# Performance work log

Measured on AMD Instinct MI355X. Metric: run time of the kernel, lower is better.

## Reference

```python
import jax, jax.numpy as jnp
import numpy as np

EPS = 1e-6

def _ln(x, w, b):
    m = x.mean(-1, keepdims=True)
    v = ((x - m) ** 2).mean(-1, keepdims=True)
    return (x - m) / jnp.sqrt(v + EPS) * w + b

def setup_inputs() -> dict:
    key = jax.random.key(0)
    ks = jax.random.split(key, 16)
    N, P, C, M = 8192, 64, 128, 4096
    MW = M * P  # 262144 gathered tokens
    A, BL = 131072, 65536
    x = jax.random.normal(ks[0], (N, P, C), dtype=jnp.float32)
    index_window = jax.random.permutation(ks[1], N)[:M]
    index_partition = jax.random.permutation(ks[2], MW)
    perm2 = jax.random.permutation(ks[3], MW)
    asy_index = perm2[:A]
    blocked_index = perm2[A:A + BL]
    p = lambda k, sh: 0.02 * jax.random.normal(k, sh, dtype=jnp.float32)
    return {
        "x": x,
        "index_window": index_window,
        "index_partition": index_partition,
        "asy_index": asy_index,
        "blocked_index": blocked_index,
        "M": M,
        "B": N,
        "ln1_w": jnp.ones((C,), jnp.float32), "ln1_b": jnp.zeros((C,), jnp.float32),
        "qkv_w": p(ks[4], (C, 3 * C)), "qkv_b": jnp.zeros((3 * C,), jnp.float32),
        "proj_w": p(ks[5], (C, C)), "proj_b": jnp.zeros((C,), jnp.float32),
        "gamma1": jnp.full((C,), 1e-1, jnp.float32),
        "ln2_w": jnp.ones((C,), jnp.float32), "ln2_b": jnp.zeros((C,), jnp.float32),
        "mlp_w1": p(ks[6], (C, 4 * C)), "mlp_b1": jnp.zeros((4 * C,), jnp.float32),
        "mlp_w2": p(ks[7], (4 * C, C)), "mlp_b2": jnp.zeros((C,), jnp.float32),
        "gamma2": jnp.full((C,), 1e-1, jnp.float32),
    }

def reference(x, index_window, index_partition, asy_index, blocked_index, M, B,
              ln1_w, ln1_b, qkv_w, qkv_b, proj_w, proj_b, gamma1,
              ln2_w, ln2_b, mlp_w1, mlp_b1, mlp_w2, mlp_b2, gamma2):
    N, P, C = x.shape
    H, dh = 4, 32
    scale = dh ** -0.5
    MW = index_partition.shape[0]
    x = _ln(x, ln1_w, ln1_b)                      # first_norm over whole input
    X = x                                          # (N, P, C)
    xw = x[index_window].reshape(-1, C)            # gather windows -> (MW, C)
    XX = xw
    xa = _ln(xw[asy_index], ln1_w, ln1_b)          # second norm on asy tokens
    xw = xw.at[asy_index].set(xa)
    shortcut = xa                                  # (A, C)
    xp = xw[index_partition].reshape(M, -1, C)     # (M, P, C) attention groups
    qkv = (xp @ qkv_w + qkv_b).reshape(M, P, H, 3 * dh).transpose(0, 2, 1, 3)
    q, k, v = jnp.split(qkv, 3, axis=3)            # each (M, H, P, dh)
    attn = jnp.einsum('mhqd,mhkd->mhqk', q, k) * scale
    # scatter scores keyed by key-token into flat map, mask blocked keys, gather back
    am = jnp.zeros((MW, P, H), attn.dtype)
    am = am.at[index_partition].set(jnp.transpose(attn, (0, 3, 2, 1)).reshape(MW, P, H))
    am = am.at[blocked_index].set(-10000.0)
    attn = jnp.transpose(am[index_partition].reshape(M, P, P, H), (0, 3, 2, 1))
    attn = jax.nn.softmax(attn, axis=-1)
    o = jnp.einsum('mhqk,mhkd->mhqd', attn, v).transpose(0, 2, 1, 3).reshape(M, P, C)
    o = o @ proj_w + proj_b
    XX = XX.at[index_partition].set(o.reshape(-1, C))
    y = XX[asy_index]
    # sub_layers: [ls1, droppath(id), ln2, mlp, ls2, droppath(id)]
    y = y * gamma1                                 # i=0
    y = shortcut + y                               # i=1 residual
    shortcut = y
    y2 = _ln(y, ln2_w, ln2_b)                      # i=2
    y2 = jax.nn.gelu(y2 @ mlp_w1 + mlp_b1, approximate=False) @ mlp_w2 + mlp_b2  # i=3
    y2 = y2 * gamma2                               # i=4
    y = shortcut + y2                              # i=5 residual
    XX = XX.at[asy_index].set(y)
    XX = XX.at[blocked_index].set(X[index_window].reshape(-1, C)[blocked_index])
    X = X.at[index_window].set(XX.reshape(M, -1, C))
    return X
```

## Files before the change

### kernel.cpp

```cpp
#include <hip/hip_runtime.h>
#include <hip/hip_bf16.h>
#include <math.h>

#define N_   8192
#define P_   64
#define C_   128
#define M_   4096
#define MW_  (M_ * P_)
#define A_   131072
#define BL_  65536
#define NROWS_ (N_ * P_)

typedef __attribute__((ext_vector_type(8))) __bf16 bf16x8;
typedef __attribute__((ext_vector_type(4))) float f32x4;
typedef __attribute__((ext_vector_type(2))) __bf16 bf16x2;

__device__ __forceinline__ float wave_sum(float v) {
#pragma unroll
  for (int o = 32; o > 0; o >>= 1) v += __shfl_xor(v, o, 64);
  return v;
}

__global__ __launch_bounds__(256) void k_set8(unsigned char* p, int n) {
  int i = blockIdx.x * 256 + threadIdx.x;
  if (i < n) p[i] = 0;
}
__global__ __launch_bounds__(256) void k_scatter2(unsigned char* p,
                                                  const int* __restrict__ ia,
                                                  const int* __restrict__ ib) {
  int i = blockIdx.x * 256 + threadIdx.x;
  if (i < A_) p[ia[i]] = 1;
  else {
    int j = i - A_;
    if (j < BL_) p[ib[j]] = 2;
  }
}

__global__ __launch_bounds__(256) void k_prep(const float* __restrict__ qkvw,
                                              const float* __restrict__ projw,
                                              const float* __restrict__ w1,
                                              const float* __restrict__ w2,
                                              __bf16* __restrict__ qkvt,
                                              __bf16* __restrict__ projt,
                                              __bf16* __restrict__ w1t,
                                              __bf16* __restrict__ w2t) {
  int i = blockIdx.x * 256 + threadIdx.x;
  if (i < 384 * 128) {
    int col = i >> 7, row = i & 127;
    qkvt[i] = (__bf16)qkvw[row * 384 + col];
  } else if (i < 384 * 128 + 128 * 128) {
    int j = i - 384 * 128;
    int col = j >> 7, row = j & 127;
    projt[j] = (__bf16)projw[row * 128 + col];
  } else if (i < 384 * 128 + 128 * 128 + 512 * 128) {
    int j = i - 384 * 128 - 128 * 128;
    int col = j >> 7, row = j & 127;
    w1t[j] = (__bf16)w1[row * 512 + col];
  } else {
    int j = i - 384 * 128 - 128 * 128 - 512 * 128;
    int col = j >> 9, row = j & 511;
    w2t[j] = (__bf16)w2[row * 128 + col];
  }
}

__global__ __launch_bounds__(256) void k_ln_all(const float* __restrict__ x,
                                                const float* __restrict__ w,
                                                const float* __restrict__ b,
                                                float* __restrict__ out) {
  int hw = threadIdx.x >> 5, l = threadIdx.x & 31;
  size_t row = (size_t)blockIdx.x * 8 + hw;
  float4 v = ((const float4*)(x + row * 128))[l];
  float s = (v.x + v.y) + (v.z + v.w);
#pragma unroll
  for (int o = 1; o < 32; o <<= 1) s += __shfl_xor(s, o, 64);
  float mean = s * (1.0f / 128.0f);
  float d0 = v.x - mean, d1 = v.y - mean, d2 = v.z - mean, d3 = v.w - mean;
  float q = (d0 * d0 + d1 * d1) + (d2 * d2 + d3 * d3);
#pragma unroll
  for (int o = 1; o < 32; o <<= 1) q += __shfl_xor(q, o, 64);
  float inv = rsqrtf(q * (1.0f / 128.0f) + 1e-6f);
  float4 wv = ((const float4*)w)[l];
  float4 bv = ((const float4*)b)[l];
  float4 o4;
  o4.x = d0 * inv * wv.x + bv.x;
  o4.y = d1 * inv * wv.y + bv.y;
  o4.z = d2 * inv * wv.z + bv.z;
  o4.w = d3 * inv * wv.w + bv.w;
  ((float4*)(out + row * 128))[l] = o4;
}

__global__ __launch_bounds__(256, 3) void k_attn(
    const int* __restrict__ iw,
    const int* __restrict__ ip, const unsigned char* __restrict__ flags,
    const float* __restrict__ ln1w, const float* __restrict__ ln1b,
    const __bf16* __restrict__ qkvt, const float* __restrict__ qkvb,
    const __bf16* __restrict__ projt, const float* __restrict__ projb,
    float* out) {
  __shared__ __align__(16) __bf16 XV[64 * 132];
  __shared__ __align__(16) __bf16 scratch[4 * 4352];
  __shared__ int srow[64];
  __shared__ unsigned char fl[64];

  const int tid = threadIdx.x;
  const int w = tid >> 6, lane = tid & 63;
  const int quad = lane >> 4, cl = lane & 15;
  const int m = blockIdx.x;

  if (tid < 64) {
    int s = ip[(m << 6) + tid];
    fl[tid] = flags[s];
    srow[tid] = iw[s >> 6] * 64 + (s & 63);
  }
  __syncthreads();

  __bf16* Xs = XV;
  const float lw0 = ln1w[2 * lane], lw1 = ln1w[2 * lane + 1];
  const float lb0 = ln1b[2 * lane], lb1 = ln1b[2 * lane + 1];

  {
    float2 xv[16];
#pragma unroll
    for (int ii = 0; ii < 16; ++ii) {
      int r = w + 4 * ii;
      xv[ii] = ((const float2*)(out + (size_t)srow[r] * 128))[lane];
    }
#pragma unroll
    for (int ii = 0; ii < 16; ++ii) {
      int r = w + 4 * ii;
      float y0 = xv[ii].x, y1 = xv[ii].y;
      if (fl[r] == 1) {
        float mean = wave_sum(y0 + y1) * (1.0f / 128.0f);
        float d0 = y0 - mean, d1 = y1 - mean;
        float inv = rsqrtf(wave_sum(d0 * d0 + d1 * d1) * (1.0f / 128.0f) + 1e-6f);
        y0 = d0 * inv * lw0 + lb0;
        y1 = d1 * inv * lw1 + lb1;
      }
      bf16x2 p2;
      p2[0] = (__bf16)y0; p2[1] = (__bf16)y1;
      *(bf16x2*)&Xs[r * 132 + 2 * lane] = p2;
    }
  }
  __syncthreads();

  __bf16* wsc = scratch + w * 4352;
  __bf16* Qs  = wsc;
  __bf16* Ks  = wsc + 2176;
  __bf16* Vts = XV + w * 2112;
  __bf16* Ps  = wsc;
  __bf16* Os  = wsc;
  const int h = w;

  bf16x8 af[4][4];
#pragma unroll
  for (int mt = 0; mt < 4; ++mt)
#pragma unroll
    for (int kt = 0; kt < 4; ++kt)
      af[mt][kt] = *(const bf16x8*)&Xs[(mt * 16 + cl) * 132 + kt * 32 + quad * 8];
  __syncthreads();

#pragma unroll
  for (int t = 0; t < 3; ++t) {
#pragma unroll
    for (int nt = 0; nt < 2; ++nt) {
      int col = h * 96 + t * 32 + nt * 16 + cl;
      bf16x8 bfr[4];
#pragma unroll
      for (int kt = 0; kt < 4; ++kt)
        bfr[kt] = *(const bf16x8*)&qkvt[(size_t)col * 128 + kt * 32 + quad * 8];
      float bias = qkvb[col];
      __builtin_amdgcn_s_setprio(1);
#pragma unroll
      for (int mt = 0; mt < 4; ++mt) {
        f32x4 acc = {bias, bias, bias, bias};
#pragma unroll
        for (int kt = 0; kt < 4; ++kt)
          acc = __builtin_amdgcn_mfma_f32_16x16x32_bf16(af[mt][kt], bfr[kt], acc, 0, 0, 0);
        if (t == 0) {
#pragma unroll
          for (int r = 0; r < 4; ++r)
            Qs[(mt * 16 + quad * 4 + r) * 34 + nt * 16 + cl] = (__bf16)acc[r];
        } else if (t == 1) {
#pragma unroll
          for (int r = 0; r < 4; ++r)
            Ks[(mt * 16 + quad * 4 + r) * 34 + nt * 16 + cl] = (__bf16)acc[r];
        } else {
#pragma unroll
          for (int r = 0; r < 4; ++r)
            Vts[(nt * 16 + cl) * 66 + mt * 16 + quad * 4 + r] = (__bf16)acc[r];
        }
      }
      __builtin_amdgcn_s_setprio(0);
    }
  }

  f32x4 sc4[4][4];
  {
    bf16x8 bk[4];
#pragma unroll
    for (int nt = 0; nt < 4; ++nt)
      bk[nt] = *(const bf16x8*)&Ks[(nt * 16 + cl) * 34 + quad * 8];
    __builtin_amdgcn_s_setprio(1);
#pragma unroll
    for (int mt = 0; mt < 4; ++mt) {
      bf16x8 aq = *(const bf16x8*)&Qs[(mt * 16 + cl) * 34 + quad * 8];
#pragma unroll
      for (int nt = 0; nt < 4; ++nt) {
        f32x4 z = {0.f, 0.f, 0.f, 0.f};
        sc4[mt][nt] = __builtin_amdgcn_mfma_f32_16x16x32_bf16(aq, bk[nt], z, 0, 0, 0);
      }
    }
    __builtin_amdgcn_s_setprio(0);
  }
  const float scale = 0.17677669529663687f;
  bool blk[4];
#pragma unroll
  for (int nt = 0; nt < 4; ++nt) blk[nt] = (fl[nt * 16 + cl] == 2);
#pragma unroll
  for (int mt = 0; mt < 4; ++mt)
#pragma unroll
    for (int nt = 0; nt < 4; ++nt)
#pragma unroll
      for (int r = 0; r < 4; ++r) {
        float v = sc4[mt][nt][r];
        sc4[mt][nt][r] = blk[nt] ? -10000.0f : v * scale;
      }
#pragma unroll
  for (int mt = 0; mt < 4; ++mt) {
#pragma unroll
    for (int r = 0; r < 4; ++r) {
      float mx = fmaxf(fmaxf(sc4[mt][0][r], sc4[mt][1][r]),
                       fmaxf(sc4[mt][2][r], sc4[mt][3][r]));
#pragma unroll
      for (int off = 1; off < 16; off <<= 1) mx = fmaxf(mx, __shfl_xor(mx, off, 64));
      float e0 = __expf(sc4[mt][0][r] - mx);
      float e1 = __expf(sc4[mt][1][r] - mx);
      float e2 = __expf(sc4[mt][2][r] - mx);
      float e3 = __expf(sc4[mt][3][r] - mx);
      float sm = (e0 + e1) + (e2 + e3);
#pragma unroll
      for (int off = 1; off < 16; off <<= 1) sm += __shfl_xor(sm, off, 64);
      float inv = 1.0f / sm;
      int row = mt * 16 + quad * 4 + r;
      Ps[row * 68 +  0 + cl] = (__bf16)(e0 * inv);
      Ps[row * 68 + 16 + cl] = (__bf16)(e1 * inv);
      Ps[row * 68 + 32 + cl] = (__bf16)(e2 * inv);
      Ps[row * 68 + 48 + cl] = (__bf16)(e3 * inv);
    }
  }

  f32x4 oacc[4][2];
  {
    bf16x8 bv[2][2];
#pragma unroll
    for (int nt = 0; nt < 2; ++nt)
#pragma unroll
      for (int kt = 0; kt < 2; ++kt)
        bv[nt][kt] = *(const bf16x8*)&Vts[(nt * 16 + cl) * 66 + kt * 32 + quad * 8];
    __builtin_amdgcn_s_setprio(1);
#pragma unroll
    for (int mt = 0; mt < 4; ++mt) {
      bf16x8 ap0 = *(const bf16x8*)&Ps[(mt * 16 + cl) * 68 + quad * 8];
      bf16x8 ap1 = *(const bf16x8*)&Ps[(mt * 16 + cl) * 68 + 32 + quad * 8];
#pragma unroll
      for (int nt = 0; nt < 2; ++nt) {
        f32x4 z = {0.f, 0.f, 0.f, 0.f};
        z = __builtin_amdgcn_mfma_f32_16x16x32_bf16(ap0, bv[nt][0], z, 0, 0, 0);
        z = __builtin_amdgcn_mfma_f32_16x16x32_bf16(ap1, bv[nt][1], z, 0, 0, 0);
        oacc[mt][nt] = z;
      }
    }
    __builtin_amdgcn_s_setprio(0);
  }
#pragma unroll
  for (int mt = 0; mt < 4; ++mt)
#pragma unroll
    for (int nt = 0; nt < 2; ++nt)
#pragma unroll
      for (int r = 0; r < 4; ++r)
        Os[(mt * 16 + quad * 4 + r) * 36 + nt * 16 + cl] = (__bf16)oacc[mt][nt][r];
  __syncthreads();

  const int jw = w * 32;
#pragma unroll
  for (int mt = 0; mt < 4; ++mt) {
#pragma unroll
    for (int nt = 0; nt < 2; ++nt) {
      int col = jw + nt * 16 + cl;
      float pb = projb[col];
      f32x4 acc = {pb, pb, pb, pb};
#pragma unroll
      for (int kt = 0; kt < 4; ++kt) {
        const __bf16* op = scratch + kt * 4352;
        bf16x8 a = *(const bf16x8*)&op[(mt * 16 + cl) * 36 + quad * 8];
        bf16x8 bb = *(const bf16x8*)&projt[(size_t)col * 128 + kt * 32 + quad * 8];
        acc = __builtin_amdgcn_mfma_f32_16x16x32_bf16(a, bb, acc, 0, 0, 0);
      }
#pragma unroll
      for (int r = 0; r < 4; ++r) {
        int row = mt * 16 + quad * 4 + r;
        if (fl[row] != 2)
          out[(size_t)srow[row] * 128 + col] = acc[r];
      }
    }
  }
}

__global__ __launch_bounds__(256, 4) void k_mlp(
    const float* __restrict__ x, const int* __restrict__ iw,
    const int* __restrict__ ia,
    const float* __restrict__ ln1w, const float* __restrict__ ln1b,
    const float* __restrict__ g1,
    const float* __restrict__ ln2w, const float* __restrict__ ln2b,
    const __bf16* __restrict__ w1t, const float* __restrict__ b1,
    const __bf16* __restrict__ w2t, const float* __restrict__ b2,
    const float* __restrict__ g2,
    float* out) {
  __shared__ __align__(16) __bf16 y2s[64 * 136];
  __shared__ __align__(16) __bf16 hb[64 * 136];
  __shared__ int wrs[64];

  const int tid = threadIdx.x;
  const int w = tid >> 6, lane = tid & 63;
  const int quad = lane >> 4, cl = lane & 15;

  if (tid < 64) {
    int s = ia[(blockIdx.x << 6) + tid];
    wrs[tid] = iw[s >> 6] * 64 + (s & 63);
  }
  __syncthreads();

  const float lw0 = ln1w[2 * lane], lw1 = ln1w[2 * lane + 1];
  const float lb0 = ln1b[2 * lane], lb1 = ln1b[2 * lane + 1];
  const float g1a = g1[2 * lane], g1b = g1[2 * lane + 1];
  const float l2w0 = ln2w[2 * lane], l2w1 = ln2w[2 * lane + 1];
  const float l2b0 = ln2b[2 * lane], l2b1 = ln2b[2 * lane + 1];

  for (int half = 0; half < 2; ++half) {
    float2 xv[8], ov[8];
#pragma unroll
    for (int ii = 0; ii < 8; ++ii) {
      int r = w + 4 * (half * 8 + ii);
      size_t wr = (size_t)wrs[r];
      xv[ii] = ((const float2*)(x + wr * 128))[lane];
      ov[ii] = ((const float2*)(out + wr * 128))[lane];
    }
#pragma unroll
    for (int ii = 0; ii < 8; ++ii) {
      int r = w + 4 * (half * 8 + ii);
      float mean = wave_sum(xv[ii].x + xv[ii].y) * (1.0f / 128.0f);
      float d0 = xv[ii].x - mean, d1 = xv[ii].y - mean;
      float inv = rsqrtf(wave_sum(d0 * d0 + d1 * d1) * (1.0f / 128.0f) + 1e-6f);
      float y0 = d0 * inv * lw0 + lb0, y1 = d1 * inv * lw1 + lb1;
      mean = wave_sum(y0 + y1) * (1.0f / 128.0f);
      d0 = y0 - mean; d1 = y1 - mean;
      inv = rsqrtf(wave_sum(d0 * d0 + d1 * d1) * (1.0f / 128.0f) + 1e-6f);
      float xa0 = d0 * inv * lw0 + lb0, xa1 = d1 * inv * lw1 + lb1;
      float yv0 = xa0 + g1a * ov[ii].x;
      float yv1 = xa1 + g1b * ov[ii].y;
      ((float2*)(out + (size_t)wrs[r] * 128))[lane] = make_float2(yv0, yv1);
      mean = wave_sum(yv0 + yv1) * (1.0f / 128.0f);
      d0 = yv0 - mean; d1 = yv1 - mean;
      inv = rsqrtf(wave_sum(d0 * d0 + d1 * d1) * (1.0f / 128.0f) + 1e-6f);
      bf16x2 p2;
      p2[0] = (__bf16)(d0 * inv * l2w0 + l2b0);
      p2[1] = (__bf16)(d1 * inv * l2w1 + l2b1);
      *(bf16x2*)&y2s[r * 136 + 2 * lane] = p2;
    }
  }
  __threadfence_block();
  __syncthreads();

  f32x4 zacc[4][2];
#pragma unroll
  for (int nt = 0; nt < 2; ++nt) {
    float bb = b2[w * 32 + nt * 16 + cl];
#pragma unroll
    for (int mt = 0; mt < 4; ++mt) zacc[mt][nt] = (f32x4){bb, bb, bb, bb};
  }

  for (int ch = 0; ch < 4; ++ch) {
#pragma unroll
    for (int nt = 0; nt < 2; ++nt) {
      int col = ch * 128 + w * 32 + nt * 16 + cl;
      bf16x8 bfr[4];
#pragma unroll
      for (int kt = 0; kt < 4; ++kt)
        bfr[kt] = *(const bf16x8*)&w1t[(size_t)col * 128 + kt * 32 + quad * 8];
      float bias = b1[col];
      __builtin_amdgcn_s_setprio(1);
#pragma unroll
      for (int mt = 0; mt < 4; ++mt) {
        f32x4 acc = {bias, bias, bias, bias};
#pragma unroll
        for (int kt = 0; kt < 4; ++kt) {
          bf16x8 a = *(const bf16x8*)&y2s[(mt * 16 + cl) * 136 + kt * 32 + quad * 8];
          acc = __builtin_amdgcn_mfma_f32_16x16x32_bf16(a, bfr[kt], acc, 0, 0, 0);
        }
#pragma unroll
        for (int r = 0; r < 4; ++r) {
          float a = acc[r];
          float g = a * 0.5f * (1.0f + erff(a * 0.70710678118654752f));
          hb[(mt * 16 + quad * 4 + r) * 136 + w * 32 + nt * 16 + cl] = (__bf16)g;
        }
      }
      __builtin_amdgcn_s_setprio(0);
    }
    __syncthreads();
#pragma unroll
    for (int nt = 0; nt < 2; ++nt) {
      int col = w * 32 + nt * 16 + cl;
      bf16x8 bfr[4];
#pragma unroll
      for (int kk = 0; kk < 4; ++kk)
        bfr[kk] = *(const bf16x8*)&w2t[(size_t)col * 512 + ch * 128 + kk * 32 + quad * 8];
      __builtin_amdgcn_s_setprio(1);
#pragma unroll
      for (int mt = 0; mt < 4; ++mt)
#pragma unroll
        for (int kk = 0; kk < 4; ++kk) {
          bf16x8 a = *(const bf16x8*)&hb[(mt * 16 + cl) * 136 + kk * 32 + quad * 8];
          zacc[mt][nt] = __builtin_amdgcn_mfma_f32_16x16x32_bf16(a, bfr[kk],
                                                                zacc[mt][nt], 0, 0, 0);
        }
      __builtin_amdgcn_s_setprio(0);
    }
    __syncthreads();
  }

#pragma unroll
  for (int mt = 0; mt < 4; ++mt)
#pragma unroll
    for (int nt = 0; nt < 2; ++nt) {
      int col = w * 32 + nt * 16 + cl;
      float gg = g2[col];
#pragma unroll
      for (int r = 0; r < 4; ++r) {
        int row = mt * 16 + quad * 4 + r;
        size_t a = (size_t)wrs[row] * 128 + col;
        out[a] = out[a] + gg * zacc[mt][nt][r];
      }
    }
}

extern "C" void kernel_launch(void* const* d_in, const int* in_sizes, int n_in,
                              void* d_out, int out_size, void* d_ws, size_t ws_size,
                              hipStream_t stream) {
  const float* x = (const float*)d_in[0];
  const int* iw = (const int*)d_in[1];
  const int* ip = (const int*)d_in[2];
  const int* ia = (const int*)d_in[3];
  const int* ib = (const int*)d_in[4];
  const float* ln1w = (const float*)d_in[7];
  const float* ln1b = (const float*)d_in[8];
  const float* qkvw = (const float*)d_in[9];
  const float* qkvb = (const float*)d_in[10];
  const float* projw = (const float*)d_in[11];
  const float* projb = (const float*)d_in[12];
  const float* g1 = (const float*)d_in[13];
  const float* ln2w = (const float*)d_in[14];
  const float* ln2b = (const float*)d_in[15];
  const float* w1 = (const float*)d_in[16];
  const float* b1 = (const float*)d_in[17];
  const float* w2 = (const float*)d_in[18];
  const float* b2 = (const float*)d_in[19];
  const float* g2 = (const float*)d_in[20];
  float* out = (float*)d_out;

  unsigned char* flags = (unsigned char*)d_ws;
  __bf16* qkvt = (__bf16*)((char*)d_ws + MW_);
  __bf16* projt = (__bf16*)((char*)d_ws + MW_ + 384 * 128 * 2);
  __bf16* w1t = (__bf16*)((char*)d_ws + MW_ + 384 * 128 * 2 + 128 * 128 * 2);
  __bf16* w2t = (__bf16*)((char*)d_ws + MW_ + 384 * 128 * 2 + 128 * 128 * 2 + 512 * 128 * 2);

  k_set8<<<MW_ / 256, 256, 0, stream>>>(flags, MW_);
  k_scatter2<<<(A_ + BL_) / 256, 256, 0, stream>>>(flags, ia, ib);
  k_prep<<<(384 * 128 + 128 * 128 + 512 * 128 + 128 * 512) / 256, 256, 0, stream>>>(
      qkvw, projw, w1, w2, qkvt, projt, w1t, w2t);
  k_ln_all<<<NROWS_ / 8, 256, 0, stream>>>(x, ln1w, ln1b, out);
  k_attn<<<M_, 256, 0, stream>>>(iw, ip, flags, ln1w, ln1b, qkvt, qkvb,
                                 projt, projb, out);
  k_mlp<<<A_ / 64, 256, 0, stream>>>(x, iw, ia, ln1w, ln1b, g1, ln2w, ln2b,
                                     w1t, b1, w2t, b2, g2, out);
}
```

Before: 804.3 us.

## Split attention work across 8 waves per block with row-halves per head

The attention kernel moves from 256 to 512 threads per block, and each head's query rows are split across two waves. This halves per-wave registers and MFMA chains, which should raise occupancy and latency hiding. The projection stage now holds its weight fragments in registers, one 16-column slice per wave, instead of reloading them per row tile. In exchange it adds extra block-wide barriers, because the two waves sharing a head's Q/K/P scratch must synchronise before buffers are reused.

```diff
diff --git a/kernel.cpp b/kernel.cpp
--- a/kernel.cpp
+++ b/kernel.cpp
@@ -89,7 +89,7 @@
   ((float4*)(out + row * 128))[l] = o4;
 }
 
-__global__ __launch_bounds__(256, 3) void k_attn(
+__global__ __launch_bounds__(512, 6) void k_attn(
     const int* __restrict__ iw,
     const int* __restrict__ ip, const unsigned char* __restrict__ flags,
     const float* __restrict__ ln1w, const float* __restrict__ ln1b,
@@ -104,6 +104,7 @@
   const int tid = threadIdx.x;
   const int w = tid >> 6, lane = tid & 63;
   const int quad = lane >> 4, cl = lane & 15;
+  const int h = w >> 1, mh = w & 1;
   const int m = blockIdx.x;
 
   if (tid < 64) {
@@ -118,15 +119,15 @@
   const float lb0 = ln1b[2 * lane], lb1 = ln1b[2 * lane + 1];
 
   {
-    float2 xv[16];
-#pragma unroll
-    for (int ii = 0; ii < 16; ++ii) {
-      int r = w + 4 * ii;
+    float2 xv[8];
+#pragma unroll
+    for (int ii = 0; ii < 8; ++ii) {
+      int r = w * 8 + ii;
       xv[ii] = ((const float2*)(out + (size_t)srow[r] * 128))[lane];
     }
 #pragma unroll
-    for (int ii = 0; ii < 16; ++ii) {
-      int r = w + 4 * ii;
+    for (int ii = 0; ii < 8; ++ii) {
+      int r = w * 8 + ii;
       float y0 = xv[ii].x, y1 = xv[ii].y;
       if (fl[r] == 1) {
         float mean = wave_sum(y0 + y1) * (1.0f / 128.0f);
@@ -142,20 +143,19 @@
   }
   __syncthreads();
 
-  __bf16* wsc = scratch + w * 4352;
+  __bf16* wsc = scratch + h * 4352;
   __bf16* Qs  = wsc;
   __bf16* Ks  = wsc + 2176;
-  __bf16* Vts = XV + w * 2112;
+  __bf16* Vts = XV + h * 2112;
   __bf16* Ps  = wsc;
   __bf16* Os  = wsc;
-  const int h = w;
-
-  bf16x8 af[4][4];
-#pragma unroll
-  for (int mt = 0; mt < 4; ++mt)
+
+  bf16x8 af[2][4];
+#pragma unroll
+  for (int mtl = 0; mtl < 2; ++mtl)
 #pragma unroll
     for (int kt = 0; kt < 4; ++kt)
-      af[mt][kt] = *(const bf16x8*)&Xs[(mt * 16 + cl) * 132 + kt * 32 + quad * 8];
+      af[mtl][kt] = *(const bf16x8*)&Xs[((mh * 2 + mtl) * 16 + cl) * 132 + kt * 32 + quad * 8];
   __syncthreads();
 
 #pragma unroll
@@ -170,11 +170,12 @@
       float bias = qkvb[col];
       __builtin_amdgcn_s_setprio(1);
 #pragma unroll
-      for (int mt = 0; mt < 4; ++mt) {
+      for (int mtl = 0; mtl < 2; ++mtl) {
+        int mt = mh * 2 + mtl;
         f32x4 acc = {bias, bias, bias, bias};
 #pragma unroll
         for (int kt = 0; kt < 4; ++kt)
-          acc = __builtin_amdgcn_mfma_f32_16x16x32_bf16(af[mt][kt], bfr[kt], acc, 0, 0, 0);
+          acc = __builtin_amdgcn_mfma_f32_16x16x32_bf16(af[mtl][kt], bfr[kt], acc, 0, 0, 0);
         if (t == 0) {
 #pragma unroll
           for (int r = 0; r < 4; ++r)
@@ -192,55 +193,60 @@
       __builtin_amdgcn_s_setprio(0);
     }
   }
-
-  f32x4 sc4[4][4];
+  __syncthreads();
+
+  f32x4 sc4[2][4];
   {
     bf16x8 bk[4];
 #pragma unroll
     for (int nt = 0; nt < 4; ++nt)
       bk[nt] = *(const bf16x8*)&Ks[(nt * 16 + cl) * 34 + quad * 8];
+    bf16x8 aq[2];
+#pragma unroll
+    for (int mtl = 0; mtl < 2; ++mtl)
+      aq[mtl] = *(const bf16x8*)&Qs[((mh * 2 + mtl) * 16 + cl) * 34 + quad * 8];
     __builtin_amdgcn_s_setprio(1);
 #pragma unroll
-    for (int mt = 0; mt < 4; ++mt) {
-      bf16x8 aq = *(const bf16x8*)&Qs[(mt * 16 + cl) * 34 + quad * 8];
+    for (int mtl = 0; mtl < 2; ++mtl)
 #pragma unroll
       for (int nt = 0; nt < 4; ++nt) {
         f32x4 z = {0.f, 0.f, 0.f, 0.f};
-        sc4[mt][nt] = __builtin_amdgcn_mfma_f32_16x16x32_bf16(aq, bk[nt], z, 0, 0, 0);
-      }
-    }
+        sc4[mtl][nt] = __builtin_amdgcn_mfma_f32_16x16x32_bf16(aq[mtl], bk[nt], z, 0, 0, 0);
+      }
     __builtin_amdgcn_s_setprio(0);
   }
+  __syncthreads();
+
   const float scale = 0.17677669529663687f;
   bool blk[4];
 #pragma unroll
   for (int nt = 0; nt < 4; ++nt) blk[nt] = (fl[nt * 16 + cl] == 2);
 #pragma unroll
-  for (int mt = 0; mt < 4; ++mt)
+  for (int mtl = 0; mtl < 2; ++mtl)
 #pragma unroll
     for (int nt = 0; nt < 4; ++nt)
 #pragma unroll
       for (int r = 0; r < 4; ++r) {
-        float v = sc4[mt][nt][r];
-        sc4[mt][nt][r] = blk[nt] ? -10000.0f : v * scale;
-      }
-#pragma unroll
-  for (int mt = 0; mt < 4; ++mt) {
+        float v = sc4[mtl][nt][r];
+        sc4[mtl][nt][r] = blk[nt] ? -10000.0f : v * scale;
+      }
+#pragma unroll
+  for (int mtl = 0; mtl < 2; ++mtl) {
 #pragma unroll
     for (int r = 0; r < 4; ++r) {
-      float mx = fmaxf(fmaxf(sc4[mt][0][r], sc4[mt][1][r]),
-                       fmaxf(sc4[mt][2][r], sc4[mt][3][r]));
+      float mx = fmaxf(fmaxf(sc4[mtl][0][r], sc4[mtl][1][r]),
+                       fmaxf(sc4[mtl][2][r], sc4[mtl][3][r]));
 #pragma unroll
       for (int off = 1; off < 16; off <<= 1) mx = fmaxf(mx, __shfl_xor(mx, off, 64));
-      float e0 = __expf(sc4[mt][0][r] - mx);
-      float e1 = __expf(sc4[mt][1][r] - mx);
-      float e2 = __expf(sc4[mt][2][r] - mx);
-      float e3 = __expf(sc4[mt][3][r] - mx);
+      float e0 = __expf(sc4[mtl][0][r] - mx);
+      float e1 = __expf(sc4[mtl][1][r] - mx);
+      float e2 = __expf(sc4[mtl][2][r] - mx);
+      float e3 = __expf(sc4[mtl][3][r] - mx);
       float sm = (e0 + e1) + (e2 + e3);
 #pragma unroll
       for (int off = 1; off < 16; off <<= 1) sm += __shfl_xor(sm, off, 64);
       float inv = 1.0f / sm;
-      int row = mt * 16 + quad * 4 + r;
+      int row = (mh * 2 + mtl) * 16 + quad * 4 + r;
       Ps[row * 68 +  0 + cl] = (__bf16)(e0 * inv);
       Ps[row * 68 + 16 + cl] = (__bf16)(e1 * inv);
       Ps[row * 68 + 32 + cl] = (__bf16)(e2 * inv);
@@ -248,7 +254,7 @@
     }
   }
 
-  f32x4 oacc[4][2];
+  f32x4 oacc[2][2];
   {
     bf16x8 bv[2][2];
 #pragma unroll
@@ -258,7 +264,8 @@
         bv[nt][kt] = *(const bf16x8*)&Vts[(nt * 16 + cl) * 66 + kt * 32 + quad * 8];
     __builtin_amdgcn_s_setprio(1);
 #pragma unroll
-    for (int mt = 0; mt < 4; ++mt) {
+    for (int mtl = 0; mtl < 2; ++mtl) {
+      int mt = mh * 2 + mtl;
       bf16x8 ap0 = *(const bf16x8*)&Ps[(mt * 16 + cl) * 68 + quad * 8];
       bf16x8 ap1 = *(const bf16x8*)&Ps[(mt * 16 + cl) * 68 + 32 + quad * 8];
 #pragma unroll
@@ -266,34 +273,36 @@
         f32x4 z = {0.f, 0.f, 0.f, 0.f};
         z = __builtin_amdgcn_mfma_f32_16x16x32_bf16(ap0, bv[nt][0], z, 0, 0, 0);
         z = __builtin_amdgcn_mfma_f32_16x16x32_bf16(ap1, bv[nt][1], z, 0, 0, 0);
-        oacc[mt][nt] = z;
+        oacc[mtl][nt] = z;
       }
     }
     __builtin_amdgcn_s_setprio(0);
   }
-#pragma unroll
-  for (int mt = 0; mt < 4; ++mt)
+  __syncthreads();
+#pragma unroll
+  for (int mtl = 0; mtl < 2; ++mtl)
 #pragma unroll
     for (int nt = 0; nt < 2; ++nt)
 #pragma unroll
       for (int r = 0; r < 4; ++r)
-        Os[(mt * 16 + quad * 4 + r) * 36 + nt * 16 + cl] = (__bf16)oacc[mt][nt][r];
-  __syncthreads();
-
-  const int jw = w * 32;
-#pragma unroll
-  for (int mt = 0; mt < 4; ++mt) {
-#pragma unroll
-    for (int nt = 0; nt < 2; ++nt) {
-      int col = jw + nt * 16 + cl;
-      float pb = projb[col];
+        Os[((mh * 2 + mtl) * 16 + quad * 4 + r) * 36 + nt * 16 + cl] = (__bf16)oacc[mtl][nt][r];
+  __syncthreads();
+
+  {
+    const int col = w * 16 + cl;
+    bf16x8 bpr[4];
+#pragma unroll
+    for (int kt = 0; kt < 4; ++kt)
+      bpr[kt] = *(const bf16x8*)&projt[(size_t)col * 128 + kt * 32 + quad * 8];
+    const float pb = projb[col];
+#pragma unroll
+    for (int mt = 0; mt < 4; ++mt) {
       f32x4 acc = {pb, pb, pb, pb};
 #pragma unroll
       for (int kt = 0; kt < 4; ++kt) {
         const __bf16* op = scratch + kt * 4352;
         bf16x8 a = *(const bf16x8*)&op[(mt * 16 + cl) * 36 + quad * 8];
-        bf16x8 bb = *(const bf16x8*)&projt[(size_t)col * 128 + kt * 32 + quad * 8];
-        acc = __builtin_amdgcn_mfma_f32_16x16x32_bf16(a, bb, acc, 0, 0, 0);
+        acc = __builtin_amdgcn_mfma_f32_16x16x32_bf16(a, bpr[kt], acc, 0, 0, 0);
       }
 #pragma unroll
       for (int r = 0; r < 4; ++r) {
@@ -477,7 +486,7 @@
   k_prep<<<(384 * 128 + 128 * 128 + 512 * 128 + 128 * 512) / 256, 256, 0, stream>>>(
       qkvw, projw, w1, w2, qkvt, projt, w1t, w2t);
   k_ln_all<<<NROWS_ / 8, 256, 0, stream>>>(x, ln1w, ln1b, out);
-  k_attn<<<M_, 256, 0, stream>>>(iw, ip, flags, ln1w, ln1b, qkvt, qkvb,
+  k_attn<<<M_, 512, 0, stream>>>(iw, ip, flags, ln1w, ln1b, qkvt, qkvb,
                                  projt, projb, out);
   k_mlp<<<A_ / 64, 256, 0, stream>>>(x, iw, ia, ln1w, ln1b, g1, ln2w, ln2b,
                                      w1t, b1, w2t, b2, g2, out);
```

New measurement: 838.8 us. 4.3% more time.

## Merge weight prep into LN launch and keep MLP residual and operands on-chip

Applied to the files above, without the earlier changes.

Folds the weight transpose/convert kernel into the first-LayerNorm kernel as extra blocks, removing one launch. In the MLP kernel, the residual row is kept in shared memory instead of being written to and re-read from global memory. The two bf16 LDS buffers become one reused buffer, and the MFMA A-operands are preloaded into registers. Occupancy is lowered to 3 blocks per CU to make room for the extra registers and shared memory.

```diff
diff --git a/kernel.cpp b/kernel.cpp
--- a/kernel.cpp
+++ b/kernel.cpp
@@ -10,6 +10,8 @@
 #define A_   131072
 #define BL_  65536
 #define NROWS_ (N_ * P_)
+#define LNBLK_ (NROWS_ / 8)
+#define PREPBLK_ (196608 / 256)
 
 typedef __attribute__((ext_vector_type(8))) __bf16 bf16x8;
 typedef __attribute__((ext_vector_type(4))) float f32x4;
@@ -36,37 +38,38 @@
   }
 }
 
-__global__ __launch_bounds__(256) void k_prep(const float* __restrict__ qkvw,
-                                              const float* __restrict__ projw,
-                                              const float* __restrict__ w1,
-                                              const float* __restrict__ w2,
-                                              __bf16* __restrict__ qkvt,
-                                              __bf16* __restrict__ projt,
-                                              __bf16* __restrict__ w1t,
-                                              __bf16* __restrict__ w2t) {
-  int i = blockIdx.x * 256 + threadIdx.x;
-  if (i < 384 * 128) {
-    int col = i >> 7, row = i & 127;
-    qkvt[i] = (__bf16)qkvw[row * 384 + col];
-  } else if (i < 384 * 128 + 128 * 128) {
-    int j = i - 384 * 128;
-    int col = j >> 7, row = j & 127;
-    projt[j] = (__bf16)projw[row * 128 + col];
-  } else if (i < 384 * 128 + 128 * 128 + 512 * 128) {
-    int j = i - 384 * 128 - 128 * 128;
-    int col = j >> 7, row = j & 127;
-    w1t[j] = (__bf16)w1[row * 512 + col];
-  } else {
-    int j = i - 384 * 128 - 128 * 128 - 512 * 128;
-    int col = j >> 9, row = j & 511;
-    w2t[j] = (__bf16)w2[row * 128 + col];
-  }
-}
-
-__global__ __launch_bounds__(256) void k_ln_all(const float* __restrict__ x,
-                                                const float* __restrict__ w,
-                                                const float* __restrict__ b,
-                                                float* __restrict__ out) {
+__global__ __launch_bounds__(256) void k_ln_prep(const float* __restrict__ x,
+                                                 const float* __restrict__ w,
+                                                 const float* __restrict__ b,
+                                                 const float* __restrict__ qkvw,
+                                                 const float* __restrict__ projw,
+                                                 const float* __restrict__ w1,
+                                                 const float* __restrict__ w2,
+                                                 __bf16* __restrict__ qkvt,
+                                                 __bf16* __restrict__ projt,
+                                                 __bf16* __restrict__ w1t,
+                                                 __bf16* __restrict__ w2t,
+                                                 float* __restrict__ out) {
+  if (blockIdx.x >= LNBLK_) {
+    int i = (blockIdx.x - LNBLK_) * 256 + threadIdx.x;
+    if (i < 384 * 128) {
+      int col = i >> 7, row = i & 127;
+      qkvt[i] = (__bf16)qkvw[row * 384 + col];
+    } else if (i < 384 * 128 + 128 * 128) {
+      int j = i - 384 * 128;
+      int col = j >> 7, row = j & 127;
+      projt[j] = (__bf16)projw[row * 128 + col];
+    } else if (i < 384 * 128 + 128 * 128 + 512 * 128) {
+      int j = i - 384 * 128 - 128 * 128;
+      int col = j >> 7, row = j & 127;
+      w1t[j] = (__bf16)w1[row * 512 + col];
+    } else {
+      int j = i - 384 * 128 - 128 * 128 - 512 * 128;
+      int col = j >> 9, row = j & 511;
+      w2t[j] = (__bf16)w2[row * 128 + col];
+    }
+    return;
+  }
   int hw = threadIdx.x >> 5, l = threadIdx.x & 31;
   size_t row = (size_t)blockIdx.x * 8 + hw;
   float4 v = ((const float4*)(x + row * 128))[l];
@@ -305,7 +308,7 @@
   }
 }
 
-__global__ __launch_bounds__(256, 4) void k_mlp(
+__global__ __launch_bounds__(256, 3) void k_mlp(
     const float* __restrict__ x, const int* __restrict__ iw,
     const int* __restrict__ ia,
     const float* __restrict__ ln1w, const float* __restrict__ ln1b,
@@ -314,9 +317,9 @@
     const __bf16* __restrict__ w1t, const float* __restrict__ b1,
     const __bf16* __restrict__ w2t, const float* __restrict__ b2,
     const float* __restrict__ g2,
-    float* out) {
-  __shared__ __align__(16) __bf16 y2s[64 * 136];
-  __shared__ __align__(16) __bf16 hb[64 * 136];
+    float* __restrict__ out) {
+  __shared__ __align__(16) float ys[64][130];
+  __shared__ __align__(16) __bf16 buf[64 * 132];
   __shared__ int wrs[64];
 
   const int tid = threadIdx.x;
@@ -357,17 +360,25 @@
       float xa0 = d0 * inv * lw0 + lb0, xa1 = d1 * inv * lw1 + lb1;
       float yv0 = xa0 + g1a * ov[ii].x;
       float yv1 = xa1 + g1b * ov[ii].y;
-      ((float2*)(out + (size_t)wrs[r] * 128))[lane] = make_float2(yv0, yv1);
+      ys[r][2 * lane] = yv0;
+      ys[r][2 * lane + 1] = yv1;
       mean = wave_sum(yv0 + yv1) * (1.0f / 128.0f);
       d0 = yv0 - mean; d1 = yv1 - mean;
       inv = rsqrtf(wave_sum(d0 * d0 + d1 * d1) * (1.0f / 128.0f) + 1e-6f);
       bf16x2 p2;
       p2[0] = (__bf16)(d0 * inv * l2w0 + l2b0);
       p2[1] = (__bf16)(d1 * inv * l2w1 + l2b1);
-      *(bf16x2*)&y2s[r * 136 + 2 * lane] = p2;
-    }
-  }
-  __threadfence_block();
+      *(bf16x2*)&buf[r * 132 + 2 * lane] = p2;
+    }
+  }
+  __syncthreads();
+
+  bf16x8 af[4][4];
+#pragma unroll
+  for (int mt = 0; mt < 4; ++mt)
+#pragma unroll
+    for (int kt = 0; kt < 4; ++kt)
+      af[mt][kt] = *(const bf16x8*)&buf[(mt * 16 + cl) * 132 + kt * 32 + quad * 8];
   __syncthreads();
 
   f32x4 zacc[4][2];
@@ -392,20 +403,24 @@
       for (int mt = 0; mt < 4; ++mt) {
         f32x4 acc = {bias, bias, bias, bias};
 #pragma unroll
-        for (int kt = 0; kt < 4; ++kt) {
-          bf16x8 a = *(const bf16x8*)&y2s[(mt * 16 + cl) * 136 + kt * 32 + quad * 8];
-          acc = __builtin_amdgcn_mfma_f32_16x16x32_bf16(a, bfr[kt], acc, 0, 0, 0);
-        }
+        for (int kt = 0; kt < 4; ++kt)
+          acc = __builtin_amdgcn_mfma_f32_16x16x32_bf16(af[mt][kt], bfr[kt], acc, 0, 0, 0);
 #pragma unroll
         for (int r = 0; r < 4; ++r) {
           float a = acc[r];
           float g = a * 0.5f * (1.0f + erff(a * 0.70710678118654752f));
-          hb[(mt * 16 + quad * 4 + r) * 136 + w * 32 + nt * 16 + cl] = (__bf16)g;
+          buf[(mt * 16 + quad * 4 + r) * 132 + w * 32 + nt * 16 + cl] = (__bf16)g;
         }
       }
       __builtin_amdgcn_s_setprio(0);
     }
     __syncthreads();
+    bf16x8 ah[4][4];
+#pragma unroll
+    for (int mt = 0; mt < 4; ++mt)
+#pragma unroll
+      for (int kk = 0; kk < 4; ++kk)
+        ah[mt][kk] = *(const bf16x8*)&buf[(mt * 16 + cl) * 132 + kk * 32 + quad * 8];
 #pragma unroll
     for (int nt = 0; nt < 2; ++nt) {
       int col = w * 32 + nt * 16 + cl;
@@ -417,11 +432,9 @@
 #pragma unroll
       for (int mt = 0; mt < 4; ++mt)
 #pragma unroll
-        for (int kk = 0; kk < 4; ++kk) {
-          bf16x8 a = *(const bf16x8*)&hb[(mt * 16 + cl) * 136 + kk * 32 + quad * 8];
-          zacc[mt][nt] = __builtin_amdgcn_mfma_f32_16x16x32_bf16(a, bfr[kk],
-                                                                zacc[mt][nt], 0, 0, 0);
-        }
+        for (int kk = 0; kk < 4; ++kk)
+          zacc[mt][nt] = __builtin_amdgcn_mfma_f32_16x16x32_bf16(ah[mt][kk], bfr[kk],
+                                                                 zacc[mt][nt], 0, 0, 0);
       __builtin_amdgcn_s_setprio(0);
     }
     __syncthreads();
@@ -436,8 +449,7 @@
 #pragma unroll
       for (int r = 0; r < 4; ++r) {
         int row = mt * 16 + quad * 4 + r;
-        size_t a = (size_t)wrs[row] * 128 + col;
-        out[a] = out[a] + gg * zacc[mt][nt][r];
+        out[(size_t)wrs[row] * 128 + col] = ys[row][col] + gg * zacc[mt][nt][r];
       }
     }
 }
@@ -474,9 +486,8 @@
 
   k_set8<<<MW_ / 256, 256, 0, stream>>>(flags, MW_);
   k_scatter2<<<(A_ + BL_) / 256, 256, 0, stream>>>(flags, ia, ib);
-  k_prep<<<(384 * 128 + 128 * 128 + 512 * 128 + 128 * 512) / 256, 256, 0, stream>>>(
-      qkvw, projw, w1, w2, qkvt, projt, w1t, w2t);
-  k_ln_all<<<NROWS_ / 8, 256, 0, stream>>>(x, ln1w, ln1b, out);
+  k_ln_prep<<<LNBLK_ + PREPBLK_, 256, 0, stream>>>(x, ln1w, ln1b,
+      qkvw, projw, w1, w2, qkvt, projt, w1t, w2t, out);
   k_attn<<<M_, 256, 0, stream>>>(iw, ip, flags, ln1w, ln1b, qkvt, qkvb,
                                  projt, projb, out);
   k_mlp<<<A_ / 64, 256, 0, stream>>>(x, iw, ia, ln1w, ln1b, g1, ln2w, ln2b,
```

Measured after the change: 857.8 us. +6.7%, slower.
